# Kernel optimization log

Hardware: AMD Instinct MI355X
Metric: run time of the kernel (lower is better)

Reference implementation:

```python
import jax, jax.numpy as jnp
import numpy as np

DIM = 768
EPS = 1e-06


def _layernorm(x, gamma, beta):
    # LayerNorm over last axis (channels), eps=EPS, elementwise affine
    mu = jnp.mean(x, axis=-1, keepdims=True)
    var = jnp.mean(jnp.square(x - mu), axis=-1, keepdims=True)
    return (x - mu) * jax.lax.rsqrt(var + EPS) * gamma + beta


def setup_inputs() -> dict:
    key = jax.random.key(0)
    ks = jax.random.split(key, 10)
    B, C, H, W = 16, DIM, 32, 32
    s = 1.0 / np.sqrt(C)  # mimic Conv2d default init scale
    return {
        "x": jax.random.normal(ks[0], (B, C, H, W), dtype=jnp.float32),
        "W1": jax.random.uniform(ks[1], (C, C), jnp.float32, -s, s),
        "b1": jax.random.uniform(ks[2], (C,), jnp.float32, -s, s),
        "g1": jnp.ones((C,), jnp.float32),
        "beta1": jnp.zeros((C,), jnp.float32),
        "W2": jax.random.uniform(ks[3], (C, C), jnp.float32, -s, s),
        "b2": jax.random.uniform(ks[4], (C,), jnp.float32, -s, s),
        "g2": jnp.ones((C,), jnp.float32),
        "beta2": jnp.zeros((C,), jnp.float32),
        "W3": jax.random.uniform(ks[5], (C, C), jnp.float32, -s, s),
        "b3": jax.random.uniform(ks[6], (C,), jnp.float32, -s, s),
    }


def reference(x, W1, b1, g1, beta1, W2, b2, g2, beta2, W3, b3):
    # x: [B, C, H, W] (NCHW). Work in NHWC; 1x1 conv == channel matmul.
    h = jnp.transpose(x, (0, 2, 3, 1))  # [B, H, W, C]
    h = jnp.einsum("bhwc,oc->bhwo", h, W1) + b1
    h = jax.nn.gelu(_layernorm(h, g1, beta1), approximate=False)
    h = jnp.einsum("bhwc,oc->bhwo", h, W2) + b2
    h = jax.nn.gelu(_layernorm(h, g2, beta2), approximate=False)
    h = jnp.einsum("bhwc,oc->bhwo", h, W3) + b3
    return jnp.transpose(h, (0, 3, 1, 2))  # back to NCHW
```

## Files before the change

kernel.cpp:

```cpp
#include <hip/hip_runtime.h>
#include <hip/hip_bf16.h>

typedef __bf16 bf16;
typedef __bf16 bf16x4 __attribute__((ext_vector_type(4)));
typedef __bf16 bf16x8 __attribute__((ext_vector_type(8)));
typedef float f32x4 __attribute__((ext_vector_type(4)));

#define DIM 768
#define HW 1024
#define BATCH 16
#define M_TOTAL (BATCH * HW)

__global__ void wcvt_kernel(const float4* __restrict__ w, bf16x4* __restrict__ o) {
    int i = blockIdx.x * 256 + threadIdx.x;
    float4 v = w[i];
    bf16x4 r = { (bf16)v.x, (bf16)v.y, (bf16)v.z, (bf16)v.w };
    o[i] = r;
}

__global__ void transpose_cvt_kernel(const float* __restrict__ x, bf16* __restrict__ xb) {
    __shared__ float tile[32][33];
    const int b = blockIdx.z;
    const int hw0 = blockIdx.x * 32;
    const int c0 = blockIdx.y * 32;
    const int tx = threadIdx.x, ty = threadIdx.y;

    const float* src = x + ((size_t)b * DIM + c0) * HW + hw0;
#pragma unroll
    for (int j = 0; j < 4; j++)
        tile[ty + 8 * j][tx] = src[(size_t)(ty + 8 * j) * HW + tx];
    __syncthreads();
    bf16* dst = xb + ((size_t)b * HW + hw0) * DIM + c0;
#pragma unroll
    for (int j = 0; j < 4; j++)
        dst[(size_t)(ty + 8 * j) * DIM + tx] = (bf16)tile[tx][ty + 8 * j];
}

template <int MODE>
__global__ __launch_bounds__(256) void gemm_kernel(
    const bf16* __restrict__ A,
    const bf16* __restrict__ Bw,
    const float* __restrict__ bias,
    void* __restrict__ out)
{
    constexpr int K = DIM;
    __shared__ bf16 As[128][32];
    __shared__ bf16 Bs[128][32];

    const int t = threadIdx.x;
    const int lane = t & 63;
    const int wave = t >> 6;
    const int wr = wave >> 1, wc = wave & 1;
    const int m0 = blockIdx.x * 128;
    const int n0 = blockIdx.y * 128;

    f32x4 acc[4][4] = {};

    const int srow = t >> 2;
    const int glin = t & 3;
    const int fr = lane & 15;
    const int kb = (lane >> 4) * 4;

    const int s_rd = (fr >> 1) & 3;
    const int g0 = kb >> 3;
    const int rem = kb & 7;
    const int offLo = ((g0 ^ s_rd) << 3) + rem;
    const int offHi = (((g0 + 2) ^ s_rd) << 3) + rem;

    for (int k0 = 0; k0 < K; k0 += 32) {
#pragma unroll
        for (int i = 0; i < 2; i++) {
            const int r = srow + i * 64;
            const int gsrc = glin ^ ((r >> 1) & 3);
            __builtin_amdgcn_global_load_lds(
                (const __attribute__((address_space(1))) void*)(A + (size_t)(m0 + r) * K + k0 + gsrc * 8),
                (__attribute__((address_space(3))) void*)&As[r][glin * 8], 16, 0, 0);
            __builtin_amdgcn_global_load_lds(
                (const __attribute__((address_space(1))) void*)(Bw + (size_t)(n0 + r) * K + k0 + gsrc * 8),
                (__attribute__((address_space(3))) void*)&Bs[r][glin * 8], 16, 0, 0);
        }
        __syncthreads();

        bf16x8 aF[4], bF[4];
#pragma unroll
        for (int mi = 0; mi < 4; mi++) {
            const bf16* p = &As[wr * 64 + mi * 16 + fr][0];
            bf16x4 lo = *(const bf16x4*)(p + offLo);
            bf16x4 hi = *(const bf16x4*)(p + offHi);
            aF[mi] = __builtin_shufflevector(lo, hi, 0, 1, 2, 3, 4, 5, 6, 7);
        }
#pragma unroll
        for (int ni = 0; ni < 4; ni++) {
            const bf16* p = &Bs[wc * 64 + ni * 16 + fr][0];
            bf16x4 lo = *(const bf16x4*)(p + offLo);
            bf16x4 hi = *(const bf16x4*)(p + offHi);
            bF[ni] = __builtin_shufflevector(lo, hi, 0, 1, 2, 3, 4, 5, 6, 7);
        }
#pragma unroll
        for (int mi = 0; mi < 4; mi++)
#pragma unroll
            for (int ni = 0; ni < 4; ni++)
                acc[mi][ni] = __builtin_amdgcn_mfma_f32_16x16x32_bf16(aF[mi], bF[ni], acc[mi][ni], 0, 0, 0);
        __syncthreads();
    }

    const int fq = lane >> 4;
    if (MODE == 0) {
        bf16* o = (bf16*)out;
#pragma unroll
        for (int mi = 0; mi < 4; mi++) {
            const int row = m0 + wr * 64 + mi * 16 + fq * 4;
#pragma unroll
            for (int ni = 0; ni < 4; ni++) {
                const int col = n0 + wc * 64 + ni * 16 + fr;
                const float bv = bias[col];
#pragma unroll
                for (int r = 0; r < 4; r++)
                    o[(size_t)(row + r) * DIM + col] = (bf16)(acc[mi][ni][r] + bv);
            }
        }
    } else {
        float* o = (float*)out;
#pragma unroll
        for (int mi = 0; mi < 4; mi++) {
            const int n_base = m0 + wr * 64 + mi * 16 + fq * 4;
            const int b = n_base >> 10;
            const int hw = n_base & 1023;
#pragma unroll
            for (int ni = 0; ni < 4; ni++) {
                const int col = n0 + wc * 64 + ni * 16 + fr;
                const float bv = bias[col];
                f32x4 v = acc[mi][ni] + bv;
                *(f32x4*)(o + ((size_t)b * DIM + col) * HW + hw) = v;
            }
        }
    }
}

__global__ __launch_bounds__(256) void ln_gelu_kernel(
    bf16* __restrict__ h, const float* __restrict__ g, const float* __restrict__ beta)
{
    const int wave = threadIdx.x >> 6;
    const int lane = threadIdx.x & 63;
    const int n = blockIdx.x * 4 + wave;
    bf16* row = h + (size_t)n * DIM;

    float v[12];
    float s = 0.f, ss = 0.f;
#pragma unroll
    for (int j = 0; j < 3; j++) {
        bf16x4 x = *(const bf16x4*)(row + j * 256 + lane * 4);
#pragma unroll
        for (int i = 0; i < 4; i++) {
            float f = (float)x[i];
            v[j * 4 + i] = f;
            s += f;
            ss += f * f;
        }
    }
#pragma unroll
    for (int off = 32; off > 0; off >>= 1) {
        s += __shfl_xor(s, off);
        ss += __shfl_xor(ss, off);
    }
    const float mu = s * (1.f / DIM);
    const float var = ss * (1.f / DIM) - mu * mu;
    const float rstd = rsqrtf(var + 1e-6f);

#pragma unroll
    for (int j = 0; j < 3; j++) {
        bf16x4 r;
#pragma unroll
        for (int i = 0; i < 4; i++) {
            const int c = j * 256 + lane * 4 + i;
            float y = (v[j * 4 + i] - mu) * rstd * g[c] + beta[c];
            y = 0.5f * y * (1.f + erff(y * 0.70710678118f));
            r[i] = (bf16)y;
        }
        *(bf16x4*)(row + j * 256 + lane * 4) = r;
    }
}

extern "C" void kernel_launch(void* const* d_in, const int* in_sizes, int n_in,
                              void* d_out, int out_size, void* d_ws, size_t ws_size,
                              hipStream_t stream) {
    const float* x   = (const float*)d_in[0];
    const float* W1  = (const float*)d_in[1];
    const float* b1  = (const float*)d_in[2];
    const float* g1  = (const float*)d_in[3];
    const float* be1 = (const float*)d_in[4];
    const float* W2  = (const float*)d_in[5];
    const float* b2  = (const float*)d_in[6];
    const float* g2  = (const float*)d_in[7];
    const float* be2 = (const float*)d_in[8];
    const float* W3  = (const float*)d_in[9];
    const float* b3  = (const float*)d_in[10];
    float* out = (float*)d_out;

    bf16* Wb1  = (bf16*)d_ws;
    bf16* Wb2  = Wb1 + (size_t)DIM * DIM;
    bf16* Wb3  = Wb2 + (size_t)DIM * DIM;
    bf16* buf0 = Wb3 + (size_t)DIM * DIM;
    bf16* buf1 = buf0 + (size_t)M_TOTAL * DIM;

    wcvt_kernel<<<576, 256, 0, stream>>>((const float4*)W1, (bf16x4*)Wb1);
    wcvt_kernel<<<576, 256, 0, stream>>>((const float4*)W2, (bf16x4*)Wb2);
    wcvt_kernel<<<576, 256, 0, stream>>>((const float4*)W3, (bf16x4*)Wb3);

    transpose_cvt_kernel<<<dim3(32, 24, 16), dim3(32, 8), 0, stream>>>(x, buf0);

    dim3 ggrid(M_TOTAL / 128, DIM / 128);
    gemm_kernel<0><<<ggrid, 256, 0, stream>>>(buf0, Wb1, b1, buf1);
    ln_gelu_kernel<<<M_TOTAL / 4, 256, 0, stream>>>(buf1, g1, be1);
    gemm_kernel<0><<<ggrid, 256, 0, stream>>>(buf1, Wb2, b2, buf0);
    ln_gelu_kernel<<<M_TOTAL / 4, 256, 0, stream>>>(buf0, g2, be2);
    gemm_kernel<1><<<ggrid, 256, 0, stream>>>(buf0, Wb3, b3, out);
}
```

Baseline: 172.0 us.

## Triple-buffer GEMM LDS loads with async prefetch and merge weight conversions

The GEMM main loop now uses three LDS buffers and issues global-to-LDS loads two k-tiles ahead, waiting with explicit vmcnt counts instead of a full __syncthreads before each tile. MFMA sections are raised to higher wave priority with s_setprio. The three weight conversion launches are merged into one kernel to cut launch overhead. The cost is triple the LDS per block, which can lower occupancy, and hand-tuned waitcnt values that must match the count of issued loads.

```diff
diff --git a/kernel.cpp b/kernel.cpp
--- a/kernel.cpp
+++ b/kernel.cpp
@@ -10,9 +10,17 @@
 #define HW 1024
 #define BATCH 16
 #define M_TOTAL (BATCH * HW)
-
-__global__ void wcvt_kernel(const float4* __restrict__ w, bf16x4* __restrict__ o) {
-    int i = blockIdx.x * 256 + threadIdx.x;
+#define NT 24
+
+__global__ void wcvt3_kernel(const float4* __restrict__ w1, const float4* __restrict__ w2,
+                             const float4* __restrict__ w3,
+                             bf16x4* __restrict__ o1, bf16x4* __restrict__ o2,
+                             bf16x4* __restrict__ o3) {
+    const int b = blockIdx.x;
+    const int which = b / 576;
+    const int i = (b % 576) * 256 + threadIdx.x;
+    const float4* w = which == 0 ? w1 : which == 1 ? w2 : w3;
+    bf16x4* o = which == 0 ? o1 : which == 1 ? o2 : o3;
     float4 v = w[i];
     bf16x4 r = { (bf16)v.x, (bf16)v.y, (bf16)v.z, (bf16)v.w };
     o[i] = r;
@@ -44,8 +52,8 @@
     void* __restrict__ out)
 {
     constexpr int K = DIM;
-    __shared__ bf16 As[128][32];
-    __shared__ bf16 Bs[128][32];
+    __shared__ bf16 As[3][128][32];
+    __shared__ bf16 Bs[3][128][32];
 
     const int t = threadIdx.x;
     const int lane = t & 63;
@@ -67,41 +75,63 @@
     const int offLo = ((g0 ^ s_rd) << 3) + rem;
     const int offHi = (((g0 + 2) ^ s_rd) << 3) + rem;
 
-    for (int k0 = 0; k0 < K; k0 += 32) {
+    auto stage = [&](int kt, int buf) {
+        const int k0 = kt * 32;
 #pragma unroll
         for (int i = 0; i < 2; i++) {
             const int r = srow + i * 64;
             const int gsrc = glin ^ ((r >> 1) & 3);
             __builtin_amdgcn_global_load_lds(
                 (const __attribute__((address_space(1))) void*)(A + (size_t)(m0 + r) * K + k0 + gsrc * 8),
-                (__attribute__((address_space(3))) void*)&As[r][glin * 8], 16, 0, 0);
+                (__attribute__((address_space(3))) void*)&As[buf][r][glin * 8], 16, 0, 0);
             __builtin_amdgcn_global_load_lds(
                 (const __attribute__((address_space(1))) void*)(Bw + (size_t)(n0 + r) * K + k0 + gsrc * 8),
-                (__attribute__((address_space(3))) void*)&Bs[r][glin * 8], 16, 0, 0);
-        }
-        __syncthreads();
+                (__attribute__((address_space(3))) void*)&Bs[buf][r][glin * 8], 16, 0, 0);
+        }
+    };
+
+    stage(0, 0);
+    stage(1, 1);
+
+    int c0 = 0, c1 = 1, c2 = 2;
+    for (int kt = 0; kt < NT; ++kt) {
+        if (kt < NT - 2) {
+            stage(kt + 2, c2);
+            asm volatile("s_waitcnt vmcnt(8)" ::: "memory");
+        } else if (kt == NT - 2) {
+            asm volatile("s_waitcnt vmcnt(4)" ::: "memory");
+        } else {
+            asm volatile("s_waitcnt vmcnt(0)" ::: "memory");
+        }
+        __builtin_amdgcn_s_barrier();
+        __builtin_amdgcn_sched_barrier(0);
 
         bf16x8 aF[4], bF[4];
 #pragma unroll
         for (int mi = 0; mi < 4; mi++) {
-            const bf16* p = &As[wr * 64 + mi * 16 + fr][0];
+            const bf16* p = &As[c0][wr * 64 + mi * 16 + fr][0];
             bf16x4 lo = *(const bf16x4*)(p + offLo);
             bf16x4 hi = *(const bf16x4*)(p + offHi);
             aF[mi] = __builtin_shufflevector(lo, hi, 0, 1, 2, 3, 4, 5, 6, 7);
         }
 #pragma unroll
         for (int ni = 0; ni < 4; ni++) {
-            const bf16* p = &Bs[wc * 64 + ni * 16 + fr][0];
+            const bf16* p = &Bs[c0][wc * 64 + ni * 16 + fr][0];
             bf16x4 lo = *(const bf16x4*)(p + offLo);
             bf16x4 hi = *(const bf16x4*)(p + offHi);
             bF[ni] = __builtin_shufflevector(lo, hi, 0, 1, 2, 3, 4, 5, 6, 7);
         }
+        __builtin_amdgcn_s_setprio(1);
 #pragma unroll
         for (int mi = 0; mi < 4; mi++)
 #pragma unroll
             for (int ni = 0; ni < 4; ni++)
                 acc[mi][ni] = __builtin_amdgcn_mfma_f32_16x16x32_bf16(aF[mi], bF[ni], acc[mi][ni], 0, 0, 0);
-        __syncthreads();
+        __builtin_amdgcn_s_setprio(0);
+        __builtin_amdgcn_sched_barrier(0);
+        __builtin_amdgcn_s_barrier();
+
+        const int tmp = c0; c0 = c1; c1 = c2; c2 = tmp;
     }
 
     const int fq = lane >> 4;
@@ -203,9 +233,8 @@
     bf16* buf0 = Wb3 + (size_t)DIM * DIM;
     bf16* buf1 = buf0 + (size_t)M_TOTAL * DIM;
 
-    wcvt_kernel<<<576, 256, 0, stream>>>((const float4*)W1, (bf16x4*)Wb1);
-    wcvt_kernel<<<576, 256, 0, stream>>>((const float4*)W2, (bf16x4*)Wb2);
-    wcvt_kernel<<<576, 256, 0, stream>>>((const float4*)W3, (bf16x4*)Wb3);
+    wcvt3_kernel<<<1728, 256, 0, stream>>>((const float4*)W1, (const float4*)W2, (const float4*)W3,
+                                           (bf16x4*)Wb1, (bf16x4*)Wb2, (bf16x4*)Wb3);
 
     transpose_cvt_kernel<<<dim3(32, 24, 16), dim3(32, 8), 0, stream>>>(x, buf0);
 
```

New measurement: 171.1 us. Within noise of the previous version (-0.5%).
